# Kernel optimization log

Hardware: AMD Instinct MI355X
Metric: run time of the kernel (lower is better)

The kernel has to match this reference:

```python
import jax, jax.numpy as jnp
import numpy as np

DIM = 512
HID = 1024
E = 8          # num_experts
K = 2          # num_experts_per_tok
B, S = 4, 2048


def setup_inputs() -> dict:
    key = jax.random.key(0)
    ks = jax.random.split(key, 10)
    sd = DIM ** -0.5
    sh = HID ** -0.5
    return {
        "x": jax.random.normal(ks[0], (B, S, DIM), dtype=jnp.float32),
        "gate_w": jax.random.normal(ks[1], (E, DIM), dtype=jnp.float32) * sd,
        "biases": jnp.zeros((E,), dtype=jnp.float32),  # e_expert_biases
        # routed experts: swiglu  y = (silu(x@w1) * (x@w3)) @ w2
        "w1": jax.random.normal(ks[2], (E, DIM, HID), dtype=jnp.float32) * sd,
        "w3": jax.random.normal(ks[3], (E, DIM, HID), dtype=jnp.float32) * sd,
        "w2": jax.random.normal(ks[4], (E, HID, DIM), dtype=jnp.float32) * sh,
        # single shared expert
        "sw1": jax.random.normal(ks[5], (DIM, HID), dtype=jnp.float32) * sd,
        "sw3": jax.random.normal(ks[6], (DIM, HID), dtype=jnp.float32) * sd,
        "sw2": jax.random.normal(ks[7], (HID, DIM), dtype=jnp.float32) * sh,
    }


def reference(x, gate_w, biases, w1, w3, w2, sw1, sw3, sw2):
    Bb, Ss, D = x.shape
    xt = x.reshape(Bb * Ss, D)                      # [T, D]

    # shared expert (applied to full x)
    shared = (jax.nn.silu(xt @ sw1) * (xt @ sw3)) @ sw2  # [T, D]

    # router
    scores = xt @ gate_w.T                          # [T, E]
    # indices chosen from biased scores (aux-free load balancing)
    _, idx = jax.lax.top_k(scores + biases, K)      # [T, K] int
    # gate values are top-k of the UNBIASED scores (as in original code)
    topv, _ = jax.lax.top_k(scores, K)              # [T, K]
    p = jax.nn.sigmoid(topv)
    p = p / jnp.sum(p, axis=-1, keepdims=True)      # [T, K]

    # every expert on every token (dense-combine MoE reference)
    h = jax.nn.silu(jnp.einsum('td,edh->eth', xt, w1)) * jnp.einsum('td,edh->eth', xt, w3)
    y = jnp.einsum('eth,ehd->etd', h, w2)           # [E, T, D]

    onehot = jax.nn.one_hot(idx, E, dtype=xt.dtype)  # [T, K, E]
    comb = jnp.einsum('tk,tke->te', p, onehot)       # [T, E] combine weights
    out = jnp.einsum('te,etd->td', comb, y) + shared
    return out.reshape(Bb, Ss, D)
```

## Files before the change

kernel.cpp:

```cpp
#include <hip/hip_runtime.h>
#include <hip/hip_bf16.h>


#define Tn 8192
#define Dd 512
#define Hh 1024
#define NEx 9

typedef __attribute__((ext_vector_type(8))) short short8;
typedef __attribute__((ext_vector_type(4))) float f32x4;

#define AS1 __attribute__((address_space(1)))
#define AS3 __attribute__((address_space(3)))

#define OFF_XB   ((size_t)0)
#define OFF_W1T  (OFF_XB + (size_t)Tn * Dd * 2)
#define OFF_W3T  (OFF_W1T + (size_t)NEx * Hh * Dd * 2)
#define OFF_W2T  (OFF_W3T + (size_t)NEx * Hh * Dd * 2)
#define OFF_HBUF (OFF_W2T + (size_t)NEx * Dd * Hh * 2)
#define OFF_TOK  (OFF_HBUF + (size_t)(3 * Tn) * Hh * 2)
#define OFF_GS   (OFF_TOK + (size_t)NEx * Tn * 4)
#define OFF_CNT  (OFF_GS + (size_t)NEx * Tn * 4)
#define OFF_OFFS (OFF_CNT + 1024)

__device__ __forceinline__ ushort f2bf(float f) {
    unsigned int u = __float_as_uint(f);
    return (ushort)((u + 0x7fffu + ((u >> 16) & 1u)) >> 16);
}

__global__ __launch_bounds__(256) void trans_kernel(const float* __restrict__ srcA,
                                                    const float* __restrict__ srcS,
                                                    ushort* __restrict__ dst, int R, int C) {
    __shared__ float tile[32][33];
    int z = blockIdx.z;
    const float* src = (z < 8) ? srcA + (size_t)z * R * C : srcS;
    dst += (size_t)z * R * C;
    int c0 = blockIdx.x * 32, r0 = blockIdx.y * 32;
    int tx = threadIdx.x & 31, ty = threadIdx.x >> 5;
#pragma unroll
    for (int k = 0; k < 4; ++k)
        tile[ty + 8 * k][tx] = src[(size_t)(r0 + ty + 8 * k) * C + c0 + tx];
    __syncthreads();
#pragma unroll
    for (int k = 0; k < 4; ++k)
        dst[(size_t)(c0 + ty + 8 * k) * R + r0 + tx] = f2bf(tile[tx][ty + 8 * k]);
}

__global__ __launch_bounds__(256) void router_kernel(const float* __restrict__ x,
                                                     const float* __restrict__ gw,
                                                     const float* __restrict__ bias,
                                                     int* __restrict__ cnt,
                                                     int* __restrict__ tok,
                                                     float* __restrict__ gslot,
                                                     ushort* __restrict__ xb) {
    __shared__ int le[64];
    __shared__ float lg[64];
    __shared__ int lpos[64];
    __shared__ int lcnt[8];
    __shared__ int gbase[8];
    int tid = threadIdx.x, lane = tid & 63, wave = tid >> 6;
    if (tid < 8) lcnt[tid] = 0;
    __syncthreads();
    int t0 = blockIdx.x * 32 + wave * 8;
    for (int it = 0; it < 8; ++it) {
        int t = t0 + it;
        const float4* xr = (const float4*)(x + (size_t)t * Dd);
        float4 xa = xr[lane * 2], xc = xr[lane * 2 + 1];
        ushort4 o1, o2;
        o1.x = f2bf(xa.x); o1.y = f2bf(xa.y); o1.z = f2bf(xa.z); o1.w = f2bf(xa.w);
        o2.x = f2bf(xc.x); o2.y = f2bf(xc.y); o2.z = f2bf(xc.z); o2.w = f2bf(xc.w);
        *(ushort4*)(xb + (size_t)t * Dd + lane * 8) = o1;
        *(ushort4*)(xb + (size_t)t * Dd + lane * 8 + 4) = o2;
        float sc[8];
#pragma unroll
        for (int e = 0; e < 8; ++e) {
            const float4* gr = (const float4*)(gw + (size_t)e * Dd);
            float4 ga = gr[lane * 2], gc = gr[lane * 2 + 1];
            float s = xa.x * ga.x + xa.y * ga.y + xa.z * ga.z + xa.w * ga.w
                    + xc.x * gc.x + xc.y * gc.y + xc.z * gc.z + xc.w * gc.w;
#pragma unroll
            for (int o = 32; o > 0; o >>= 1) s += __shfl_xor(s, o);
            sc[e] = s;
        }
        if (lane == 0) {
            float b0 = -1e30f; int i0 = 0;
#pragma unroll
            for (int e = 0; e < 8; ++e) { float bv = sc[e] + bias[e]; if (bv > b0) { b0 = bv; i0 = e; } }
            float b1v = -1e30f; int i1 = (i0 == 0) ? 1 : 0;
#pragma unroll
            for (int e = 0; e < 8; ++e) if (e != i0) { float bv = sc[e] + bias[e]; if (bv > b1v) { b1v = bv; i1 = e; } }
            float v0 = -1e30f; int k0i = 0;
#pragma unroll
            for (int e = 0; e < 8; ++e) if (sc[e] > v0) { v0 = sc[e]; k0i = e; }
            float v1 = -1e30f;
#pragma unroll
            for (int e = 0; e < 8; ++e) if (e != k0i && sc[e] > v1) v1 = sc[e];
            float p0 = 1.f / (1.f + __expf(-v0));
            float p1 = 1.f / (1.f + __expf(-v1));
            float inv = 1.f / (p0 + p1);
            int ai = (wave * 8 + it) * 2;
            le[ai] = i0;     lg[ai] = p0 * inv;
            le[ai + 1] = i1; lg[ai + 1] = p1 * inv;
        }
    }
    __syncthreads();
    if (tid < 64) lpos[tid] = atomicAdd(&lcnt[le[tid]], 1);
    __syncthreads();
    if (tid < 8) gbase[tid] = atomicAdd(&cnt[tid * 32], lcnt[tid]);
    __syncthreads();
    if (tid < 64) {
        int e = le[tid];
        int dst = gbase[e] + lpos[tid];
        int t = blockIdx.x * 32 + (tid >> 1);
        tok[(size_t)e * Tn + dst] = t;
        gslot[(size_t)e * Tn + dst] = lg[tid];
    }
}

__global__ void scan_kernel(const int* cnt, int* off, int* cntc) {
    if (threadIdx.x == 0 && blockIdx.x == 0) {
        int s = 0;
        for (int e = 0; e < 8; ++e) { int c = cnt[e * 32]; cntc[e] = c; off[e] = s; s += c; }
        off[8] = s;
        cntc[8] = Tn;
    }
}

__global__ __launch_bounds__(256, 2) void stage1_kernel(
        const ushort* __restrict__ xb, const ushort* __restrict__ w1t,
        const ushort* __restrict__ w3t, const int* __restrict__ tok,
        const int* __restrict__ cntc, const int* __restrict__ off,
        ushort* __restrict__ Hbuf) {
    int e = blockIdx.z;
    int cn = cntc[e];
    int m0 = blockIdx.y * 128;
    if (m0 >= cn) return;
    int n0 = blockIdx.x * 64;
    const ushort* w1e = w1t + (size_t)e * Hh * Dd;
    const ushort* w3e = w3t + (size_t)e * Hh * Dd;

    __shared__ ushort As[128 * 64];
    __shared__ ushort B1s[64 * 64];
    __shared__ ushort B3s[64 * 64];
    __shared__ int toks[128];

    int tid = threadIdx.x;
    if (tid < 128) {
        int slot = m0 + tid;
        int sl = slot < cn ? slot : cn - 1;
        toks[tid] = (e == 8) ? sl : tok[(size_t)e * Tn + sl];
    }
    __syncthreads();

    int lane = tid & 63, wave = tid >> 6;
    int wm = (wave & 1) * 64, wn = (wave >> 1) * 32;
    int col15 = lane & 15, quad = lane >> 4;
    int lr = lane >> 3;
    int lcx = ((lane & 7) ^ lr) * 8;

    f32x4 acc1[4][2], acc3[4][2];
#pragma unroll
    for (int a = 0; a < 4; ++a)
#pragma unroll
        for (int b = 0; b < 2; ++b) {
            acc1[a][b] = (f32x4){0.f, 0.f, 0.f, 0.f};
            acc3[a][b] = (f32x4){0.f, 0.f, 0.f, 0.f};
        }

    for (int kb = 0; kb < Dd; kb += 64) {
#pragma unroll
        for (int i = 0; i < 4; ++i) {
            int cid = wave * 4 + i;
            const ushort* g = xb + (size_t)toks[cid * 8 + lr] * Dd + kb + lcx;
            __builtin_amdgcn_global_load_lds((const AS1 void*)g, (AS3 void*)(As + cid * 512), 16, 0, 0);
        }
#pragma unroll
        for (int i = 0; i < 2; ++i) {
            int cid = wave * 2 + i;
            int r = n0 + cid * 8 + lr;
            const ushort* g1 = w1e + (size_t)r * Dd + kb + lcx;
            const ushort* g3 = w3e + (size_t)r * Dd + kb + lcx;
            __builtin_amdgcn_global_load_lds((const AS1 void*)g1, (AS3 void*)(B1s + cid * 512), 16, 0, 0);
            __builtin_amdgcn_global_load_lds((const AS1 void*)g3, (AS3 void*)(B3s + cid * 512), 16, 0, 0);
        }
        __syncthreads();
#pragma unroll
        for (int ks = 0; ks < 2; ++ks) {
            int px = ((ks * 4 + quad) ^ (col15 & 7)) * 8;
            short8 a[4], b1[2], b3[2];
#pragma unroll
            for (int mi = 0; mi < 4; ++mi)
                a[mi] = *(const short8*)&As[(wm + mi * 16 + col15) * 64 + px];
#pragma unroll
            for (int ni = 0; ni < 2; ++ni) {
                b1[ni] = *(const short8*)&B1s[(wn + ni * 16 + col15) * 64 + px];
                b3[ni] = *(const short8*)&B3s[(wn + ni * 16 + col15) * 64 + px];
            }
#pragma unroll
            for (int mi = 0; mi < 4; ++mi)
#pragma unroll
                for (int ni = 0; ni < 2; ++ni) {
                    acc1[mi][ni] = __builtin_amdgcn_mfma_f32_16x16x32_bf16(a[mi], b1[ni], acc1[mi][ni], 0, 0, 0);
                    acc3[mi][ni] = __builtin_amdgcn_mfma_f32_16x16x32_bf16(a[mi], b3[ni], acc3[mi][ni], 0, 0, 0);
                }
        }
        __syncthreads();
    }

    int oe = off[e];
#pragma unroll
    for (int mi = 0; mi < 4; ++mi)
#pragma unroll
        for (int r = 0; r < 4; ++r) {
            int slot = m0 + wm + mi * 16 + quad * 4 + r;
            if (slot < cn) {
                size_t rowb = (size_t)(oe + slot) * Hh;
#pragma unroll
                for (int ni = 0; ni < 2; ++ni) {
                    float h1 = acc1[mi][ni][r], h3 = acc3[mi][ni][r];
                    float s = h1 / (1.f + __expf(-h1));
                    Hbuf[rowb + n0 + wn + ni * 16 + col15] = f2bf(s * h3);
                }
            }
        }
}

__global__ __launch_bounds__(256, 2) void stage2_kernel(
        const ushort* __restrict__ Hbuf, const ushort* __restrict__ w2t,
        const int* __restrict__ tok, const float* __restrict__ gslot,
        const int* __restrict__ cntc, const int* __restrict__ off,
        float* __restrict__ out) {
    int e = blockIdx.z;
    int cn = cntc[e];
    int m0 = blockIdx.y * 128;
    if (m0 >= cn) return;
    int n0 = blockIdx.x * 64;
    int oe = off[e];
    const ushort* w2e = w2t + (size_t)e * Dd * Hh;

    __shared__ ushort As[128 * 64];
    __shared__ ushort Bs[64 * 64];

    int tid = threadIdx.x;
    int lane = tid & 63, wave = tid >> 6;
    int wm = (wave & 1) * 64, wn = (wave >> 1) * 32;
    int col15 = lane & 15, quad = lane >> 4;
    int lr = lane >> 3;
    int lcx = ((lane & 7) ^ lr) * 8;

    f32x4 acc[4][2];
#pragma unroll
    for (int a = 0; a < 4; ++a)
#pragma unroll
        for (int b = 0; b < 2; ++b) acc[a][b] = (f32x4){0.f, 0.f, 0.f, 0.f};

    for (int kb = 0; kb < Hh; kb += 64) {
#pragma unroll
        for (int i = 0; i < 4; ++i) {
            int cid = wave * 4 + i;
            const ushort* g = Hbuf + (size_t)(oe + m0 + cid * 8 + lr) * Hh + kb + lcx;
            __builtin_amdgcn_global_load_lds((const AS1 void*)g, (AS3 void*)(As + cid * 512), 16, 0, 0);
        }
#pragma unroll
        for (int i = 0; i < 2; ++i) {
            int cid = wave * 2 + i;
            const ushort* g = w2e + (size_t)(n0 + cid * 8 + lr) * Hh + kb + lcx;
            __builtin_amdgcn_global_load_lds((const AS1 void*)g, (AS3 void*)(Bs + cid * 512), 16, 0, 0);
        }
        __syncthreads();
#pragma unroll
        for (int ks = 0; ks < 2; ++ks) {
            int px = ((ks * 4 + quad) ^ (col15 & 7)) * 8;
            short8 a[4], b[2];
#pragma unroll
            for (int mi = 0; mi < 4; ++mi)
                a[mi] = *(const short8*)&As[(wm + mi * 16 + col15) * 64 + px];
#pragma unroll
            for (int ni = 0; ni < 2; ++ni)
                b[ni] = *(const short8*)&Bs[(wn + ni * 16 + col15) * 64 + px];
#pragma unroll
            for (int mi = 0; mi < 4; ++mi)
#pragma unroll
                for (int ni = 0; ni < 2; ++ni)
                    acc[mi][ni] = __builtin_amdgcn_mfma_f32_16x16x32_bf16(a[mi], b[ni], acc[mi][ni], 0, 0, 0);
        }
        __syncthreads();
    }

#pragma unroll
    for (int mi = 0; mi < 4; ++mi)
#pragma unroll
        for (int r = 0; r < 4; ++r) {
            int slot = m0 + wm + mi * 16 + quad * 4 + r;
            if (slot < cn) {
                int t = (e == 8) ? slot : tok[(size_t)e * Tn + slot];
                float g = (e == 8) ? 1.f : gslot[(size_t)e * Tn + slot];
#pragma unroll
                for (int ni = 0; ni < 2; ++ni)
                    atomicAdd(&out[(size_t)t * Dd + n0 + wn + ni * 16 + col15], g * acc[mi][ni][r]);
            }
        }
}

extern "C" void kernel_launch(void* const* d_in, const int* in_sizes, int n_in,
                              void* d_out, int out_size, void* d_ws, size_t ws_size,
                              hipStream_t stream) {
    (void)in_sizes; (void)n_in; (void)out_size; (void)ws_size;
    const float* x    = (const float*)d_in[0];
    const float* gw   = (const float*)d_in[1];
    const float* bias = (const float*)d_in[2];
    const float* w1   = (const float*)d_in[3];
    const float* w3   = (const float*)d_in[4];
    const float* w2   = (const float*)d_in[5];
    const float* sw1  = (const float*)d_in[6];
    const float* sw3  = (const float*)d_in[7];
    const float* sw2  = (const float*)d_in[8];
    float* out = (float*)d_out;

    char* ws = (char*)d_ws;
    ushort* xb    = (ushort*)(ws + OFF_XB);
    ushort* w1t   = (ushort*)(ws + OFF_W1T);
    ushort* w3t   = (ushort*)(ws + OFF_W3T);
    ushort* w2t   = (ushort*)(ws + OFF_W2T);
    ushort* Hbuf  = (ushort*)(ws + OFF_HBUF);
    int*    tok   = (int*)(ws + OFF_TOK);
    float*  gslot = (float*)(ws + OFF_GS);
    int*    cnt   = (int*)(ws + OFF_CNT);
    int*    off   = (int*)(ws + OFF_OFFS);
    int*    cntc  = off + 16;

    hipMemsetAsync(cnt, 0, 1024, stream);
    hipMemsetAsync(out, 0, (size_t)Tn * Dd * 4, stream);

    trans_kernel<<<dim3(32, 16, 9), 256, 0, stream>>>(w1, sw1, w1t, Dd, Hh);
    trans_kernel<<<dim3(32, 16, 9), 256, 0, stream>>>(w3, sw3, w3t, Dd, Hh);
    trans_kernel<<<dim3(16, 32, 9), 256, 0, stream>>>(w2, sw2, w2t, Hh, Dd);

    router_kernel<<<256, 256, 0, stream>>>(x, gw, bias, cnt, tok, gslot, xb);
    scan_kernel<<<1, 64, 0, stream>>>(cnt, off, cntc);

    stage1_kernel<<<dim3(Hh / 64, 64, NEx), 256, 0, stream>>>(xb, w1t, w3t, tok, cntc, off, Hbuf);
    stage2_kernel<<<dim3(Dd / 64, 64, NEx), 256, 0, stream>>>(Hbuf, w2t, tok, gslot, cntc, off, out);
}
```

Before: 286.3 us.

## Replace atomic scatter-add with bf16 expert outputs and a gather combine kernel

Stage2 now writes each expert's rows as bf16 into a compact buffer that reuses the x workspace, instead of doing fp32 atomicAdd into the output. A new combine kernel gathers the two routed rows plus the shared-expert row per token, applies the gate weights and writes the output once, so the output memset is no longer needed. The grid dimensions are also swapped so that m-tiles vary along x, which changes block scheduling order. This removes atomic contention and read-modify-write traffic, at the cost of an extra kernel launch, a bf16 rounding step on the expert outputs, and a dependence on slot indices fitting in 16 bits.

```diff
diff --git a/kernel.cpp b/kernel.cpp
--- a/kernel.cpp
+++ b/kernel.cpp
@@ -13,19 +13,24 @@
 #define AS1 __attribute__((address_space(1)))
 #define AS3 __attribute__((address_space(3)))
 
-#define OFF_XB   ((size_t)0)
-#define OFF_W1T  (OFF_XB + (size_t)Tn * Dd * 2)
-#define OFF_W3T  (OFF_W1T + (size_t)NEx * Hh * Dd * 2)
-#define OFF_W2T  (OFF_W3T + (size_t)NEx * Hh * Dd * 2)
-#define OFF_HBUF (OFF_W2T + (size_t)NEx * Dd * Hh * 2)
-#define OFF_TOK  (OFF_HBUF + (size_t)(3 * Tn) * Hh * 2)
-#define OFF_GS   (OFF_TOK + (size_t)NEx * Tn * 4)
-#define OFF_CNT  (OFF_GS + (size_t)NEx * Tn * 4)
-#define OFF_OFFS (OFF_CNT + 1024)
+#define OFF_XB    ((size_t)0)
+#define OFF_W1T   (OFF_XB + (size_t)Tn * Dd * 2)
+#define OFF_W3T   (OFF_W1T + (size_t)NEx * Hh * Dd * 2)
+#define OFF_W2T   (OFF_W3T + (size_t)NEx * Hh * Dd * 2)
+#define OFF_HBUF  (OFF_W2T + (size_t)NEx * Dd * Hh * 2)
+#define OFF_TOK   (OFF_HBUF + (size_t)(3 * Tn) * Hh * 2)
+#define OFF_SLOTP (OFF_TOK + (size_t)8 * Tn * 4)
+#define OFF_PG    (OFF_SLOTP + (size_t)Tn * 2 * 4)
+#define OFF_CNT   (OFF_PG + (size_t)Tn * 2 * 4)
+#define OFF_OFFS  (OFF_CNT + 1024)
+#define OFF_YC    OFF_XB
 
 __device__ __forceinline__ ushort f2bf(float f) {
     unsigned int u = __float_as_uint(f);
     return (ushort)((u + 0x7fffu + ((u >> 16) & 1u)) >> 16);
+}
+__device__ __forceinline__ float bf2f(short s) {
+    return __uint_as_float(((unsigned int)(unsigned short)s) << 16);
 }
 
 __global__ __launch_bounds__(256) void trans_kernel(const float* __restrict__ srcA,
@@ -51,7 +56,8 @@
                                                      const float* __restrict__ bias,
                                                      int* __restrict__ cnt,
                                                      int* __restrict__ tok,
-                                                     float* __restrict__ gslot,
+                                                     int* __restrict__ slotp,
+                                                     float* __restrict__ pg,
                                                      ushort* __restrict__ xb) {
     __shared__ int le[64];
     __shared__ float lg[64];
@@ -113,7 +119,8 @@
         int dst = gbase[e] + lpos[tid];
         int t = blockIdx.x * 32 + (tid >> 1);
         tok[(size_t)e * Tn + dst] = t;
-        gslot[(size_t)e * Tn + dst] = lg[tid];
+        slotp[t * 2 + (tid & 1)] = (e << 16) | dst;
+        pg[t * 2 + (tid & 1)] = lg[tid];
     }
 }
 
@@ -133,9 +140,9 @@
         ushort* __restrict__ Hbuf) {
     int e = blockIdx.z;
     int cn = cntc[e];
-    int m0 = blockIdx.y * 128;
+    int m0 = blockIdx.x * 128;
     if (m0 >= cn) return;
-    int n0 = blockIdx.x * 64;
+    int n0 = blockIdx.y * 64;
     const ushort* w1e = w1t + (size_t)e * Hh * Dd;
     const ushort* w3e = w3t + (size_t)e * Hh * Dd;
 
@@ -227,14 +234,13 @@
 
 __global__ __launch_bounds__(256, 2) void stage2_kernel(
         const ushort* __restrict__ Hbuf, const ushort* __restrict__ w2t,
-        const int* __restrict__ tok, const float* __restrict__ gslot,
         const int* __restrict__ cntc, const int* __restrict__ off,
-        float* __restrict__ out) {
+        ushort* __restrict__ Yc) {
     int e = blockIdx.z;
     int cn = cntc[e];
-    int m0 = blockIdx.y * 128;
+    int m0 = blockIdx.x * 128;
     if (m0 >= cn) return;
-    int n0 = blockIdx.x * 64;
+    int n0 = blockIdx.y * 64;
     int oe = off[e];
     const ushort* w2e = w2t + (size_t)e * Dd * Hh;
 
@@ -293,13 +299,35 @@
         for (int r = 0; r < 4; ++r) {
             int slot = m0 + wm + mi * 16 + quad * 4 + r;
             if (slot < cn) {
-                int t = (e == 8) ? slot : tok[(size_t)e * Tn + slot];
-                float g = (e == 8) ? 1.f : gslot[(size_t)e * Tn + slot];
+                size_t rowb = (size_t)(oe + slot) * Dd;
 #pragma unroll
                 for (int ni = 0; ni < 2; ++ni)
-                    atomicAdd(&out[(size_t)t * Dd + n0 + wn + ni * 16 + col15], g * acc[mi][ni][r]);
+                    Yc[rowb + n0 + wn + ni * 16 + col15] = f2bf(acc[mi][ni][r]);
             }
         }
+}
+
+__global__ __launch_bounds__(256) void combine_kernel(const ushort* __restrict__ Yc,
+        const int* __restrict__ slotp, const float* __restrict__ pg,
+        const int* __restrict__ off, float* __restrict__ out) {
+    int g = blockIdx.x * 256 + threadIdx.x;
+    int t = g >> 6;
+    int c = (g & 63) * 8;
+    int p0 = slotp[t * 2], p1 = slotp[t * 2 + 1];
+    float g0 = pg[t * 2], g1 = pg[t * 2 + 1];
+    int s0 = off[p0 >> 16] + (p0 & 0xffff);
+    int s1 = off[p1 >> 16] + (p1 & 0xffff);
+    int s2 = off[8] + t;
+    short8 a = *(const short8*)(Yc + (size_t)s0 * Dd + c);
+    short8 b = *(const short8*)(Yc + (size_t)s1 * Dd + c);
+    short8 d = *(const short8*)(Yc + (size_t)s2 * Dd + c);
+    float o[8];
+#pragma unroll
+    for (int i = 0; i < 8; ++i)
+        o[i] = g0 * bf2f(a[i]) + g1 * bf2f(b[i]) + bf2f(d[i]);
+    float* dst = out + (size_t)t * Dd + c;
+    *(float4*)dst = (float4){o[0], o[1], o[2], o[3]};
+    *(float4*)(dst + 4) = (float4){o[4], o[5], o[6], o[7]};
 }
 
 extern "C" void kernel_launch(void* const* d_in, const int* in_sizes, int n_in,
@@ -323,22 +351,24 @@
     ushort* w3t   = (ushort*)(ws + OFF_W3T);
     ushort* w2t   = (ushort*)(ws + OFF_W2T);
     ushort* Hbuf  = (ushort*)(ws + OFF_HBUF);
+    ushort* Yc    = (ushort*)(ws + OFF_YC);
     int*    tok   = (int*)(ws + OFF_TOK);
-    float*  gslot = (float*)(ws + OFF_GS);
+    int*    slotp = (int*)(ws + OFF_SLOTP);
+    float*  pg    = (float*)(ws + OFF_PG);
     int*    cnt   = (int*)(ws + OFF_CNT);
     int*    off   = (int*)(ws + OFF_OFFS);
     int*    cntc  = off + 16;
 
     hipMemsetAsync(cnt, 0, 1024, stream);
-    hipMemsetAsync(out, 0, (size_t)Tn * Dd * 4, stream);
 
     trans_kernel<<<dim3(32, 16, 9), 256, 0, stream>>>(w1, sw1, w1t, Dd, Hh);
     trans_kernel<<<dim3(32, 16, 9), 256, 0, stream>>>(w3, sw3, w3t, Dd, Hh);
     trans_kernel<<<dim3(16, 32, 9), 256, 0, stream>>>(w2, sw2, w2t, Hh, Dd);
 
-    router_kernel<<<256, 256, 0, stream>>>(x, gw, bias, cnt, tok, gslot, xb);
+    router_kernel<<<256, 256, 0, stream>>>(x, gw, bias, cnt, tok, slotp, pg, xb);
     scan_kernel<<<1, 64, 0, stream>>>(cnt, off, cntc);
 
-    stage1_kernel<<<dim3(Hh / 64, 64, NEx), 256, 0, stream>>>(xb, w1t, w3t, tok, cntc, off, Hbuf);
-    stage2_kernel<<<dim3(Dd / 64, 64, NEx), 256, 0, stream>>>(Hbuf, w2t, tok, gslot, cntc, off, out);
-}
+    stage1_kernel<<<dim3(64, Hh / 64, NEx), 256, 0, stream>>>(xb, w1t, w3t, tok, cntc, off, Hbuf);
+    stage2_kernel<<<dim3(64, Dd / 64, NEx), 256, 0, stream>>>(Hbuf, w2t, cntc, off, Yc);
+    combine_kernel<<<2048, 256, 0, stream>>>(Yc, slotp, pg, off, out);
+}
```

Result: faster. 273.5 us (-4.5%).
